# Optimization experiments

Measured on AMD Instinct MI355X. Metric: run time of the kernel, lower is better.

## Reference

```python
import jax, jax.numpy as jnp
import numpy as np

I1, I2, N = 256, 256, 256  # inp1_size, inp2_size, n_neurons
B = 4096
IN_DIM = (I1 + 1) * (I2 + 1)


def setup_inputs() -> dict:
    key = jax.random.key(0)
    k1, k2, kw1, kb1, kw2, kb2 = jax.random.split(key, 6)
    inp1 = jax.random.normal(k1, (B, I1), dtype=jnp.float32)
    inp2 = jax.random.normal(k2, (B, I2), dtype=jnp.float32)
    # Kaiming-uniform-ish init like torch nn.Linear
    lim1 = 1.0 / np.sqrt(IN_DIM)
    W1 = jax.random.uniform(kw1, (IN_DIM, N), jnp.float32, -lim1, lim1)
    b1 = jax.random.uniform(kb1, (N,), jnp.float32, -lim1, lim1)
    lim2 = 1.0 / np.sqrt(N)
    W2 = jax.random.uniform(kw2, (N, N), jnp.float32, -lim2, lim2)
    b2 = jax.random.uniform(kb2, (N,), jnp.float32, -lim2, lim2)
    return {"inp1": inp1, "inp2": inp2, "W1": W1, "b1": b1, "W2": W2, "b2": b2}


def reference(inp1, inp2, W1, b1, W2, b2):
    bsz = inp1.shape[0]
    ones = jnp.ones((bsz, 1), dtype=inp1.dtype)
    a = jnp.concatenate([inp1, ones], axis=-1)  # [B, I1+1]
    b = jnp.concatenate([inp2, ones], axis=-1)  # [B, I2+1]
    fusion = jnp.einsum('bi,bj->bij', a, b).reshape(bsz, -1)  # [B, (I1+1)*(I2+1)]
    h = jax.nn.relu(fusion @ W1 + b1)
    out = jax.nn.relu(h @ W2 + b2)
    return out
```

## Files before the change

kernel.cpp:

```cpp
#include <hip/hip_runtime.h>

#define DEVI __device__ __forceinline__

typedef __attribute__((ext_vector_type(4))) float f32x4;
typedef __attribute__((ext_vector_type(8))) short bf16x8;
typedef __attribute__((ext_vector_type(4))) unsigned int u32x4;

typedef __attribute__((address_space(3))) unsigned int lds_u32_t;
typedef __attribute__((address_space(1))) unsigned int glb_u32_t;

constexpr int BATCH = 4096;
constexpr int KTOT  = 66048;
constexpr size_t OFF_WPT  = 0;
constexpr size_t OFF_W2BT = 33816576;
constexpr size_t OFF_B1P  = OFF_W2BT + 131072;
constexpr size_t OFF_HF   = OFF_B1P + 1024;
constexpr size_t OFF_HB   = OFF_HF + 4194304;

DEVI unsigned int f2bf_u(float x) {
  unsigned int u = __float_as_uint(x);
  return (u + 0x7FFFu + ((u >> 16) & 1u)) >> 16;
}
DEVI unsigned int pack2(float a, float b) { return f2bf_u(a) | (f2bf_u(b) << 16); }

__global__ __launch_bounds__(256) void k_repack(const float* __restrict__ W1,
                                                unsigned short* __restrict__ wpt) {
  __shared__ float tile[64][65];
  int kt = blockIdx.x, nt = blockIdx.y, t = threadIdx.x;
  {
    int r = t >> 2, c4 = (t & 3) * 16;
    int kp = kt * 64 + r;
    int src;
    if (kp < 65536)      src = (kp >> 8) * 257 + (kp & 255);
    else if (kp < 65792) src = (kp - 65536) * 257 + 256;
    else                 src = kp;
    const float* rp = W1 + (size_t)src * 256 + nt * 64 + c4;
#pragma unroll
    for (int q = 0; q < 4; ++q) {
      f32x4 x = *(const f32x4*)(rp + q * 4);
#pragma unroll
      for (int e = 0; e < 4; ++e) tile[r][c4 + q * 4 + e] = x[e];
    }
  }
  __syncthreads();
  {
    int nl = t >> 2, kk = (t & 3) * 16;
    int n = nt * 64 + nl;
    u32x4 lo, hi;
#pragma unroll
    for (int m = 0; m < 4; ++m)
      lo[m] = pack2(tile[kk + 2 * m][nl], tile[kk + 2 * m + 1][nl]);
#pragma unroll
    for (int m = 0; m < 4; ++m)
      hi[m] = pack2(tile[kk + 8 + 2 * m][nl], tile[kk + 9 + 2 * m][nl]);
    unsigned short* dst = wpt + (size_t)n * KTOT + kt * 64 + kk;
    *(u32x4*)dst = lo;
    *(u32x4*)(dst + 8) = hi;
  }
}

__global__ __launch_bounds__(256) void k_misc(const float* __restrict__ W1,
                                              const float* __restrict__ b1,
                                              const float* __restrict__ W2,
                                              float* __restrict__ hf,
                                              unsigned short* __restrict__ w2bt,
                                              float* __restrict__ b1p) {
  int idx = blockIdx.x * 256 + threadIdx.x;
  hf[idx] = 0.f;
  if (idx < 65536) {
    int n2 = idx >> 8, n = idx & 255;
    w2bt[idx] = (unsigned short)f2bf_u(W2[n * 256 + n2]);
  }
  if (idx < 256) b1p[idx] = b1[idx] + W1[(size_t)66048 * 256 + idx];
}

DEVI void mfma_tiles(const char* A_lds, const char* W_lds, f32x4 (&acc)[8][4],
                     int lane, int wr, int wc) {
  int r16 = lane & 15;
  int kq = lane >> 4;
#pragma unroll
  for (int ks = 0; ks < 2; ++ks) {
    int kun = ks * 4 + kq;
    bf16x8 a[8];
#pragma unroll
    for (int rg = 0; rg < 8; ++rg) {
      int row = wr * 128 + rg * 16 + r16;
      a[rg] = *(const bf16x8*)(A_lds + row * 128 + ((kun ^ (row & 7)) << 4));
    }
#pragma unroll
    for (int cg = 0; cg < 4; ++cg) {
      int n = wc * 64 + cg * 16 + r16;
      bf16x8 bfr = *(const bf16x8*)(W_lds + n * 128 + ((kun ^ (n & 7)) << 4));
#pragma unroll
      for (int rg = 0; rg < 8; ++rg)
        acc[rg][cg] = __builtin_amdgcn_mfma_f32_16x16x32_bf16(a[rg], bfr, acc[rg][cg], 0, 0, 0);
    }
  }
}

DEVI void stage_w(const unsigned short* __restrict__ wpt, char* W_lds, int k0,
                  int w, int lane) {
#pragma unroll
  for (int sI = 0; sI < 4; ++sI) {
    int g = w * 256 + sI * 64 + lane;
    int n = g >> 3, u = g & 7;
    size_t gb = (size_t)n * (KTOT * 2) + (size_t)((k0 + ((u ^ (n & 7)) << 3)) * 2);
    __builtin_amdgcn_global_load_lds((const glb_u32_t*)((const char*)wpt + gb),
                                     (lds_u32_t*)(W_lds + g * 16), 16, 0, 0);
  }
}

__global__ __launch_bounds__(512) void k_main(const float* __restrict__ inp1,
                                              const float* __restrict__ inp2,
                                              const unsigned short* __restrict__ wpt,
                                              float* __restrict__ hf) {
  __shared__ u32x4 smem[4096];
  char* A_lds = (char*)smem;
  char* W_lds = (char*)smem + 32768;

  int lin = blockIdx.x;
  int xcd = lin & 7, slot = lin >> 3;
  int c = xcd + ((slot >> 4) << 3);
  int bblk = slot & 15;
  int b0 = bblk * 256;
  int i0 = c * 16;

  int t = threadIdx.x;
  int lane = t & 63, w = t >> 6;
  int wr = w >> 2, wc = w & 3;

  int row_a = t >> 1;
  int ub = (t & 1) * 4;

  const float* inp1_row = inp1 + (size_t)(b0 + row_a) * 256;
  const float* inp2_row = inp2 + (size_t)(b0 + row_a) * 256;

  f32x4 acc[8][4] = {};

  for (int js = 0; js < 4; ++js) {
    float v[32];
    {
      const f32x4* p = (const f32x4*)(inp2_row + js * 64 + ub * 8);
#pragma unroll
      for (int q = 0; q < 8; ++q) {
        f32x4 x = p[q];
#pragma unroll
        for (int e = 0; e < 4; ++e) v[q * 4 + e] = x[e];
      }
    }
    for (int ii = 0; ii < 16; ++ii) {
      int i = i0 + ii;
      float s = inp1_row[i];
#pragma unroll
      for (int uu = 0; uu < 4; ++uu) {
        int u = ub + uu;
        u32x4 pk;
#pragma unroll
        for (int m = 0; m < 4; ++m)
          pk[m] = pack2(v[uu * 8 + 2 * m] * s, v[uu * 8 + 2 * m + 1] * s);
        *(u32x4*)(A_lds + row_a * 128 + ((u ^ (row_a & 7)) << 4)) = pk;
      }
      stage_w(wpt, W_lds, i * 256 + js * 64, w, lane);
      __syncthreads();
      mfma_tiles(A_lds, W_lds, acc, lane, wr, wc);
      __syncthreads();
    }
  }

  if (c == 15) {
    for (int jt = 0; jt < 8; ++jt) {
#pragma unroll
      for (int uu = 0; uu < 4; ++uu) {
        int u = ub + uu;
        int koff = jt * 64 + u * 8;
        const float* src = (koff < 256) ? (inp1_row + koff) : (inp2_row + (koff - 256));
        f32x4 x0 = *(const f32x4*)src;
        f32x4 x1 = *(const f32x4*)(src + 4);
        u32x4 pk;
        pk[0] = pack2(x0[0], x0[1]);
        pk[1] = pack2(x0[2], x0[3]);
        pk[2] = pack2(x1[0], x1[1]);
        pk[3] = pack2(x1[2], x1[3]);
        *(u32x4*)(A_lds + row_a * 128 + ((u ^ (row_a & 7)) << 4)) = pk;
      }
      stage_w(wpt, W_lds, 65536 + jt * 64, w, lane);
      __syncthreads();
      mfma_tiles(A_lds, W_lds, acc, lane, wr, wc);
      __syncthreads();
    }
  }

#pragma unroll
  for (int rg = 0; rg < 8; ++rg)
#pragma unroll
    for (int cg = 0; cg < 4; ++cg) {
      int n = wc * 64 + cg * 16 + (lane & 15);
      int brow = b0 + wr * 128 + rg * 16 + (lane >> 4) * 4;
#pragma unroll
      for (int r = 0; r < 4; ++r)
        atomicAdd(hf + (size_t)(brow + r) * 256 + n, acc[rg][cg][r]);
    }
}

__global__ __launch_bounds__(256) void k_finalize(const float* __restrict__ hf,
                                                  const float* __restrict__ b1p,
                                                  unsigned short* __restrict__ hb) {
  int idx = blockIdx.x * 256 + threadIdx.x;
  float v = hf[idx] + b1p[idx & 255];
  hb[idx] = (unsigned short)f2bf_u(v > 0.f ? v : 0.f);
}

__global__ __launch_bounds__(256) void k_gemm2(const unsigned short* __restrict__ hb,
                                               const unsigned short* __restrict__ w2bt,
                                               const float* __restrict__ b2,
                                               float* __restrict__ out) {
  int b0 = blockIdx.x * 128, n0 = blockIdx.y * 128;
  int t = threadIdx.x, lane = t & 63, w = t >> 6;
  int wr = w >> 1, wc = w & 1;
  int r16 = lane & 15, k8 = (lane >> 4) * 8;
  f32x4 acc[4][4] = {};
  for (int ks = 0; ks < 8; ++ks) {
    int k = ks * 32 + k8;
    bf16x8 a[4], bb[4];
#pragma unroll
    for (int rg = 0; rg < 4; ++rg) {
      int b_ = b0 + wr * 64 + rg * 16 + r16;
      a[rg] = *(const bf16x8*)(hb + (size_t)b_ * 256 + k);
    }
#pragma unroll
    for (int cg = 0; cg < 4; ++cg) {
      int n2 = n0 + wc * 64 + cg * 16 + r16;
      bb[cg] = *(const bf16x8*)(w2bt + (size_t)n2 * 256 + k);
    }
#pragma unroll
    for (int rg = 0; rg < 4; ++rg)
#pragma unroll
      for (int cg = 0; cg < 4; ++cg)
        acc[rg][cg] = __builtin_amdgcn_mfma_f32_16x16x32_bf16(a[rg], bb[cg], acc[rg][cg], 0, 0, 0);
  }
#pragma unroll
  for (int rg = 0; rg < 4; ++rg)
#pragma unroll
    for (int cg = 0; cg < 4; ++cg) {
      int n2 = n0 + wc * 64 + cg * 16 + r16;
      float bias = b2[n2];
      int brow = b0 + wr * 64 + rg * 16 + (lane >> 4) * 4;
#pragma unroll
      for (int r = 0; r < 4; ++r) {
        float val = acc[rg][cg][r] + bias;
        out[(size_t)(brow + r) * 256 + n2] = val > 0.f ? val : 0.f;
      }
    }
}

extern "C" void kernel_launch(void* const* d_in, const int* in_sizes, int n_in,
                              void* d_out, int out_size, void* d_ws, size_t ws_size,
                              hipStream_t stream) {
  const float* inp1 = (const float*)d_in[0];
  const float* inp2 = (const float*)d_in[1];
  const float* W1   = (const float*)d_in[2];
  const float* b1   = (const float*)d_in[3];
  const float* W2   = (const float*)d_in[4];
  const float* b2   = (const float*)d_in[5];
  float* out = (float*)d_out;

  char* ws = (char*)d_ws;
  unsigned short* wpt  = (unsigned short*)(ws + OFF_WPT);
  unsigned short* w2bt = (unsigned short*)(ws + OFF_W2BT);
  float* b1p = (float*)(ws + OFF_B1P);
  float* hf  = (float*)(ws + OFF_HF);
  unsigned short* hb = (unsigned short*)(ws + OFF_HB);

  k_repack<<<dim3(1032, 4), 256, 0, stream>>>(W1, wpt);
  k_misc<<<4096, 256, 0, stream>>>(W1, b1, W2, hf, w2bt, b1p);
  k_main<<<256, 512, 0, stream>>>(inp1, inp2, wpt, hf);
  k_finalize<<<4096, 256, 0, stream>>>(hf, b1p, hb);
  k_gemm2<<<dim3(32, 2), 256, 0, stream>>>(hb, w2bt, b2, out);
}
```

Measured before the change: 338.0 us.

## Double-buffer LDS stages and spread tail K-chunks across blocks

```diff
diff --git a/kernel.cpp b/kernel.cpp
--- a/kernel.cpp
+++ b/kernel.cpp
@@ -9,7 +9,6 @@
 typedef __attribute__((address_space(3))) unsigned int lds_u32_t;
 typedef __attribute__((address_space(1))) unsigned int glb_u32_t;
 
-constexpr int BATCH = 4096;
 constexpr int KTOT  = 66048;
 constexpr size_t OFF_WPT  = 0;
 constexpr size_t OFF_W2BT = 33816576;
@@ -114,9 +113,8 @@
                                               const float* __restrict__ inp2,
                                               const unsigned short* __restrict__ wpt,
                                               float* __restrict__ hf) {
-  __shared__ u32x4 smem[4096];
-  char* A_lds = (char*)smem;
-  char* W_lds = (char*)smem + 32768;
+  __shared__ u32x4 smem[8192];
+  char* base = (char*)smem;
 
   int lin = blockIdx.x;
   int xcd = lin & 7, slot = lin >> 3;
@@ -135,59 +133,91 @@
   const float* inp1_row = inp1 + (size_t)(b0 + row_a) * 256;
   const float* inp2_row = inp2 + (size_t)(b0 + row_a) * 256;
 
+  float s1[16];
+  {
+    const f32x4* p = (const f32x4*)(inp1_row + i0);
+#pragma unroll
+    for (int q = 0; q < 4; ++q) {
+      f32x4 x = p[q];
+#pragma unroll
+      for (int e = 0; e < 4; ++e) s1[q * 4 + e] = x[e];
+    }
+  }
+
+  float v[32];
+  int js_cur = -1;
+  auto loadv = [&](int js) {
+    const f32x4* p = (const f32x4*)(inp2_row + js * 64 + ub * 8);
+#pragma unroll
+    for (int q = 0; q < 8; ++q) {
+      f32x4 x = p[q];
+#pragma unroll
+      for (int e = 0; e < 4; ++e) v[q * 4 + e] = x[e];
+    }
+    js_cur = js;
+  };
+
+  auto build_main = [&](char* A_lds, int ii) {
+    float s = s1[ii];
+#pragma unroll
+    for (int uu = 0; uu < 4; ++uu) {
+      int u = ub + uu;
+      u32x4 pk;
+#pragma unroll
+      for (int m = 0; m < 4; ++m)
+        pk[m] = pack2(v[uu * 8 + 2 * m] * s, v[uu * 8 + 2 * m + 1] * s);
+      *(u32x4*)(A_lds + row_a * 128 + ((u ^ (row_a & 7)) << 4)) = pk;
+    }
+  };
+
+  auto build_tail = [&](char* A_lds, int jt) {
+#pragma unroll
+    for (int uu = 0; uu < 4; ++uu) {
+      int u = ub + uu;
+      int koff = jt * 64 + u * 8;
+      const float* src = (koff < 256) ? (inp1_row + koff) : (inp2_row + (koff - 256));
+      f32x4 x0 = *(const f32x4*)src;
+      f32x4 x1 = *(const f32x4*)(src + 4);
+      u32x4 pk;
+      pk[0] = pack2(x0[0], x0[1]);
+      pk[1] = pack2(x0[2], x0[3]);
+      pk[2] = pack2(x1[0], x1[1]);
+      pk[3] = pack2(x1[2], x1[3]);
+      *(u32x4*)(A_lds + row_a * 128 + ((u ^ (row_a & 7)) << 4)) = pk;
+    }
+  };
+
   f32x4 acc[8][4] = {};
 
-  for (int js = 0; js < 4; ++js) {
-    float v[32];
-    {
-      const f32x4* p = (const f32x4*)(inp2_row + js * 64 + ub * 8);
-#pragma unroll
-      for (int q = 0; q < 8; ++q) {
-        f32x4 x = p[q];
-#pragma unroll
-        for (int e = 0; e < 4; ++e) v[q * 4 + e] = x[e];
+  const int NS = 64 + (c >= 8 ? 1 : 0);
+
+  loadv(0);
+  stage_w(wpt, base + 32768, i0 * 256, w, lane);
+  build_main(base, 0);
+  __syncthreads();
+
+  for (int s = 0; s < NS; ++s) {
+    int cur = s & 1, nxt = cur ^ 1;
+    char* A_cur = base + cur * 65536;
+    char* W_cur = base + cur * 65536 + 32768;
+    char* A_nxt = base + nxt * 65536;
+    char* W_nxt = base + nxt * 65536 + 32768;
+
+    int sn = s + 1;
+    if (sn < NS) {
+      if (sn < 64) {
+        int js = sn >> 4, ii = sn & 15;
+        stage_w(wpt, W_nxt, (i0 + ii) * 256 + js * 64, w, lane);
+        if (js != js_cur) loadv(js);
+        build_main(A_nxt, ii);
+      } else {
+        stage_w(wpt, W_nxt, 65536 + (c - 8) * 64, w, lane);
+        build_tail(A_nxt, c - 8);
       }
     }
-    for (int ii = 0; ii < 16; ++ii) {
-      int i = i0 + ii;
-      float s = inp1_row[i];
-#pragma unroll
-      for (int uu = 0; uu < 4; ++uu) {
-        int u = ub + uu;
-        u32x4 pk;
-#pragma unroll
-        for (int m = 0; m < 4; ++m)
-          pk[m] = pack2(v[uu * 8 + 2 * m] * s, v[uu * 8 + 2 * m + 1] * s);
-        *(u32x4*)(A_lds + row_a * 128 + ((u ^ (row_a & 7)) << 4)) = pk;
-      }
-      stage_w(wpt, W_lds, i * 256 + js * 64, w, lane);
-      __syncthreads();
-      mfma_tiles(A_lds, W_lds, acc, lane, wr, wc);
-      __syncthreads();
-    }
-  }
-
-  if (c == 15) {
-    for (int jt = 0; jt < 8; ++jt) {
-#pragma unroll
-      for (int uu = 0; uu < 4; ++uu) {
-        int u = ub + uu;
-        int koff = jt * 64 + u * 8;
-        const float* src = (koff < 256) ? (inp1_row + koff) : (inp2_row + (koff - 256));
-        f32x4 x0 = *(const f32x4*)src;
-        f32x4 x1 = *(const f32x4*)(src + 4);
-        u32x4 pk;
-        pk[0] = pack2(x0[0], x0[1]);
-        pk[1] = pack2(x0[2], x0[3]);
-        pk[2] = pack2(x1[0], x1[1]);
-        pk[3] = pack2(x1[2], x1[3]);
-        *(u32x4*)(A_lds + row_a * 128 + ((u ^ (row_a & 7)) << 4)) = pk;
-      }
-      stage_w(wpt, W_lds, 65536 + jt * 64, w, lane);
-      __syncthreads();
-      mfma_tiles(A_lds, W_lds, acc, lane, wr, wc);
-      __syncthreads();
-    }
+
+    mfma_tiles(A_cur, W_cur, acc, lane, wr, wc);
+    __syncthreads();
   }
 
 #pragma unroll
```

New measurement: 310.4 us. -8.2%, faster.

## Double-buffer k_main with smaller tiles, more blocks and split tail work

Applied to the files above, without the earlier changes.

```diff
diff --git a/kernel.cpp b/kernel.cpp
--- a/kernel.cpp
+++ b/kernel.cpp
@@ -9,7 +9,6 @@
 typedef __attribute__((address_space(3))) unsigned int lds_u32_t;
 typedef __attribute__((address_space(1))) unsigned int glb_u32_t;
 
-constexpr int BATCH = 4096;
 constexpr int KTOT  = 66048;
 constexpr size_t OFF_WPT  = 0;
 constexpr size_t OFF_W2BT = 33816576;
@@ -74,128 +73,138 @@
   if (idx < 256) b1p[idx] = b1[idx] + W1[(size_t)66048 * 256 + idx];
 }
 
-DEVI void mfma_tiles(const char* A_lds, const char* W_lds, f32x4 (&acc)[8][4],
-                     int lane, int wr, int wc) {
-  int r16 = lane & 15;
-  int kq = lane >> 4;
-#pragma unroll
-  for (int ks = 0; ks < 2; ++ks) {
-    int kun = ks * 4 + kq;
-    bf16x8 a[8];
-#pragma unroll
-    for (int rg = 0; rg < 8; ++rg) {
-      int row = wr * 128 + rg * 16 + r16;
-      a[rg] = *(const bf16x8*)(A_lds + row * 128 + ((kun ^ (row & 7)) << 4));
-    }
-#pragma unroll
-    for (int cg = 0; cg < 4; ++cg) {
-      int n = wc * 64 + cg * 16 + r16;
-      bf16x8 bfr = *(const bf16x8*)(W_lds + n * 128 + ((kun ^ (n & 7)) << 4));
-#pragma unroll
-      for (int rg = 0; rg < 8; ++rg)
-        acc[rg][cg] = __builtin_amdgcn_mfma_f32_16x16x32_bf16(a[rg], bfr, acc[rg][cg], 0, 0, 0);
-    }
-  }
-}
-
-DEVI void stage_w(const unsigned short* __restrict__ wpt, char* W_lds, int k0,
-                  int w, int lane) {
-#pragma unroll
-  for (int sI = 0; sI < 4; ++sI) {
-    int g = w * 256 + sI * 64 + lane;
-    int n = g >> 3, u = g & 7;
-    size_t gb = (size_t)n * (KTOT * 2) + (size_t)((k0 + ((u ^ (n & 7)) << 3)) * 2);
-    __builtin_amdgcn_global_load_lds((const glb_u32_t*)((const char*)wpt + gb),
-                                     (lds_u32_t*)(W_lds + g * 16), 16, 0, 0);
-  }
-}
-
-__global__ __launch_bounds__(512) void k_main(const float* __restrict__ inp1,
-                                              const float* __restrict__ inp2,
-                                              const unsigned short* __restrict__ wpt,
-                                              float* __restrict__ hf) {
-  __shared__ u32x4 smem[4096];
-  char* A_lds = (char*)smem;
-  char* W_lds = (char*)smem + 32768;
+__global__ __launch_bounds__(512, 4) void k_main(const float* __restrict__ inp1,
+                                                 const float* __restrict__ inp2,
+                                                 const unsigned short* __restrict__ wpt,
+                                                 float* __restrict__ hf) {
+  __shared__ char smem[49152];
 
   int lin = blockIdx.x;
   int xcd = lin & 7, slot = lin >> 3;
-  int c = xcd + ((slot >> 4) << 3);
-  int bblk = slot & 15;
-  int b0 = bblk * 256;
+  int c = xcd + ((slot >> 5) << 3);
+  int bblk = slot & 31;
+  int b0 = bblk * 128;
   int i0 = c * 16;
 
   int t = threadIdx.x;
   int lane = t & 63, w = t >> 6;
   int wr = w >> 2, wc = w & 3;
-
-  int row_a = t >> 1;
-  int ub = (t & 1) * 4;
+  int r16 = lane & 15, kun = lane >> 4;
+
+  int row_a = t >> 2;
+  int u_a = t & 3;
+  int a_waddr = row_a * 64 + ((u_a ^ ((row_a >> 1) & 3)) << 4);
 
   const float* inp1_row = inp1 + (size_t)(b0 + row_a) * 256;
   const float* inp2_row = inp2 + (size_t)(b0 + row_a) * 256;
 
-  f32x4 acc[8][4] = {};
-
-  for (int js = 0; js < 4; ++js) {
-    float v[32];
+  char* A0 = smem;             char* W0 = smem + 8192;
+  char* A1 = smem + 24576;     char* W1b = smem + 24576 + 8192;
+
+  float v[16];
+  auto loadv = [&](int js) {
+    const float* p = inp2_row + js * 64 + u_a * 8;
+#pragma unroll
+    for (int jw = 0; jw < 2; ++jw) {
+      f32x4 x0 = *(const f32x4*)(p + jw * 32);
+      f32x4 x1 = *(const f32x4*)(p + jw * 32 + 4);
+#pragma unroll
+      for (int e = 0; e < 4; ++e) { v[jw * 8 + e] = x0[e]; v[jw * 8 + 4 + e] = x1[e]; }
+    }
+  };
+
+  auto build_main = [&](char* A, int ii, int jw) {
+    float s = inp1_row[i0 + ii];
+    u32x4 pk;
+#pragma unroll
+    for (int m = 0; m < 4; ++m)
+      pk[m] = pack2(v[jw * 8 + 2 * m] * s, v[jw * 8 + 2 * m + 1] * s);
+    *(u32x4*)(A + a_waddr) = pk;
+  };
+
+  auto build_tail = [&](char* A) {
+    int koff = c * 32 + u_a * 8;
+    const float* src = (koff < 256) ? (inp1_row + koff) : (inp2_row + (koff - 256));
+    f32x4 x0 = *(const f32x4*)src;
+    f32x4 x1 = *(const f32x4*)(src + 4);
+    u32x4 pk;
+    pk[0] = pack2(x0[0], x0[1]);
+    pk[1] = pack2(x0[2], x0[3]);
+    pk[2] = pack2(x1[0], x1[1]);
+    pk[3] = pack2(x1[2], x1[3]);
+    *(u32x4*)(A + a_waddr) = pk;
+  };
+
+  auto stage = [&](char* W, int k0) {
+#pragma unroll
+    for (int sI = 0; sI < 2; ++sI) {
+      int g = w * 128 + sI * 64 + lane;
+      int n = g >> 2, u = g & 3;
+      size_t gb = (size_t)n * (KTOT * 2) +
+                  (size_t)((k0 + ((u ^ ((n >> 1) & 3)) << 3)) * 2);
+      __builtin_amdgcn_global_load_lds((const glb_u32_t*)((const char*)wpt + gb),
+                                       (lds_u32_t*)(W + g * 16), 16, 0, 0);
+    }
+  };
+
+  f32x4 acc[4][4] = {};
+
+  auto mfma_step = [&](const char* A, const char* W) {
+    bf16x8 a[4], b[4];
+#pragma unroll
+    for (int rg = 0; rg < 4; ++rg) {
+      int row = wr * 64 + rg * 16 + r16;
+      a[rg] = *(const bf16x8*)(A + row * 64 + ((kun ^ ((row >> 1) & 3)) << 4));
+    }
+#pragma unroll
+    for (int cg = 0; cg < 4; ++cg) {
+      int n = wc * 64 + cg * 16 + r16;
+      b[cg] = *(const bf16x8*)(W + n * 64 + ((kun ^ ((n >> 1) & 3)) << 4));
+    }
+#pragma unroll
+    for (int rg = 0; rg < 4; ++rg)
+#pragma unroll
+      for (int cg = 0; cg < 4; ++cg)
+        acc[rg][cg] = __builtin_amdgcn_mfma_f32_16x16x32_bf16(a[rg], b[cg], acc[rg][cg], 0, 0, 0);
+  };
+
+  loadv(0);
+  stage(W0, i0 * 256);
+  build_main(A0, 0, 0);
+  __syncthreads();
+
+  for (int s2 = 0; s2 < 64; ++s2) {
     {
-      const f32x4* p = (const f32x4*)(inp2_row + js * 64 + ub * 8);
-#pragma unroll
-      for (int q = 0; q < 8; ++q) {
-        f32x4 x = p[q];
-#pragma unroll
-        for (int e = 0; e < 4; ++e) v[q * 4 + e] = x[e];
+      int sn = 2 * s2 + 1;
+      int js = sn >> 5, ii = (sn >> 1) & 15;
+      stage(W1b, (i0 + ii) * 256 + js * 64 + 32);
+      build_main(A1, ii, 1);
+      mfma_step(A0, W0);
+      __syncthreads();
+    }
+    {
+      int sn = 2 * s2 + 2;
+      if (sn < 128) {
+        int js = sn >> 5, ii = (sn >> 1) & 15;
+        stage(W0, (i0 + ii) * 256 + js * 64);
+        if ((sn & 31) == 0) loadv(js);
+        build_main(A0, ii, 0);
+      } else {
+        stage(W0, 65536 + c * 32);
+        build_tail(A0);
       }
-    }
-    for (int ii = 0; ii < 16; ++ii) {
-      int i = i0 + ii;
-      float s = inp1_row[i];
-#pragma unroll
-      for (int uu = 0; uu < 4; ++uu) {
-        int u = ub + uu;
-        u32x4 pk;
-#pragma unroll
-        for (int m = 0; m < 4; ++m)
-          pk[m] = pack2(v[uu * 8 + 2 * m] * s, v[uu * 8 + 2 * m + 1] * s);
-        *(u32x4*)(A_lds + row_a * 128 + ((u ^ (row_a & 7)) << 4)) = pk;
-      }
-      stage_w(wpt, W_lds, i * 256 + js * 64, w, lane);
+      mfma_step(A1, W1b);
       __syncthreads();
-      mfma_tiles(A_lds, W_lds, acc, lane, wr, wc);
-      __syncthreads();
-    }
-  }
-
-  if (c == 15) {
-    for (int jt = 0; jt < 8; ++jt) {
-#pragma unroll
-      for (int uu = 0; uu < 4; ++uu) {
-        int u = ub + uu;
-        int koff = jt * 64 + u * 8;
-        const float* src = (koff < 256) ? (inp1_row + koff) : (inp2_row + (koff - 256));
-        f32x4 x0 = *(const f32x4*)src;
-        f32x4 x1 = *(const f32x4*)(src + 4);
-        u32x4 pk;
-        pk[0] = pack2(x0[0], x0[1]);
-        pk[1] = pack2(x0[2], x0[3]);
-        pk[2] = pack2(x1[0], x1[1]);
-        pk[3] = pack2(x1[2], x1[3]);
-        *(u32x4*)(A_lds + row_a * 128 + ((u ^ (row_a & 7)) << 4)) = pk;
-      }
-      stage_w(wpt, W_lds, 65536 + jt * 64, w, lane);
-      __syncthreads();
-      mfma_tiles(A_lds, W_lds, acc, lane, wr, wc);
-      __syncthreads();
-    }
-  }
-
-#pragma unroll
-  for (int rg = 0; rg < 8; ++rg)
-#pragma unroll
-    for (int cg = 0; cg < 4; ++cg) {
-      int n = wc * 64 + cg * 16 + (lane & 15);
-      int brow = b0 + wr * 128 + rg * 16 + (lane >> 4) * 4;
+    }
+  }
+  mfma_step(A0, W0);
+
+#pragma unroll
+  for (int rg = 0; rg < 4; ++rg)
+#pragma unroll
+    for (int cg = 0; cg < 4; ++cg) {
+      int n = wc * 64 + cg * 16 + r16;
+      int brow = b0 + wr * 64 + rg * 16 + kun * 4;
 #pragma unroll
       for (int r = 0; r < 4; ++r)
         atomicAdd(hf + (size_t)(brow + r) * 256 + n, acc[rg][cg][r]);
@@ -273,7 +282,7 @@
 
   k_repack<<<dim3(1032, 4), 256, 0, stream>>>(W1, wpt);
   k_misc<<<4096, 256, 0, stream>>>(W1, b1, W2, hf, w2bt, b1p);
-  k_main<<<256, 512, 0, stream>>>(inp1, inp2, wpt, hf);
+  k_main<<<512, 512, 0, stream>>>(inp1, inp2, wpt, hf);
   k_finalize<<<4096, 256, 0, stream>>>(hf, b1p, hb);
   k_gemm2<<<dim3(32, 2), 256, 0, stream>>>(hb, w2bt, b2, out);
 }
```

Result: faster. 324.9 us (-3.9%).

## Double-buffer main GEMM LDS tiles with four-phase MFMA pipeline and spread tail

Applied to the files above, without the earlier changes.

```diff
diff --git a/kernel.cpp b/kernel.cpp
--- a/kernel.cpp
+++ b/kernel.cpp
@@ -1,4 +1,5 @@
 #include <hip/hip_runtime.h>
+#include <hip/hip_bf16.h>
 
 #define DEVI __device__ __forceinline__
 
@@ -9,7 +10,6 @@
 typedef __attribute__((address_space(3))) unsigned int lds_u32_t;
 typedef __attribute__((address_space(1))) unsigned int glb_u32_t;
 
-constexpr int BATCH = 4096;
 constexpr int KTOT  = 66048;
 constexpr size_t OFF_WPT  = 0;
 constexpr size_t OFF_W2BT = 33816576;
@@ -17,11 +17,13 @@
 constexpr size_t OFF_HF   = OFF_B1P + 1024;
 constexpr size_t OFF_HB   = OFF_HF + 4194304;
 
-DEVI unsigned int f2bf_u(float x) {
-  unsigned int u = __float_as_uint(x);
-  return (u + 0x7FFFu + ((u >> 16) & 1u)) >> 16;
-}
-DEVI unsigned int pack2(float a, float b) { return f2bf_u(a) | (f2bf_u(b) << 16); }
+DEVI unsigned short f2bf(float x) {
+  __hip_bfloat16 h = __float2bfloat16(x);
+  return *reinterpret_cast<unsigned short*>(&h);
+}
+DEVI unsigned int pack2(float a, float b) {
+  return (unsigned int)f2bf(a) | ((unsigned int)f2bf(b) << 16);
+}
 
 __global__ __launch_bounds__(256) void k_repack(const float* __restrict__ W1,
                                                 unsigned short* __restrict__ wpt) {
@@ -69,137 +71,199 @@
   hf[idx] = 0.f;
   if (idx < 65536) {
     int n2 = idx >> 8, n = idx & 255;
-    w2bt[idx] = (unsigned short)f2bf_u(W2[n * 256 + n2]);
+    w2bt[idx] = f2bf(W2[n * 256 + n2]);
   }
   if (idx < 256) b1p[idx] = b1[idx] + W1[(size_t)66048 * 256 + idx];
 }
 
-DEVI void mfma_tiles(const char* A_lds, const char* W_lds, f32x4 (&acc)[8][4],
-                     int lane, int wr, int wc) {
-  int r16 = lane & 15;
-  int kq = lane >> 4;
-#pragma unroll
-  for (int ks = 0; ks < 2; ++ks) {
-    int kun = ks * 4 + kq;
-    bf16x8 a[8];
-#pragma unroll
-    for (int rg = 0; rg < 8; ++rg) {
-      int row = wr * 128 + rg * 16 + r16;
-      a[rg] = *(const bf16x8*)(A_lds + row * 128 + ((kun ^ (row & 7)) << 4));
-    }
+__global__ __launch_bounds__(512, 2) void k_main(const float* __restrict__ inp1,
+                                                 const float* __restrict__ inp2,
+                                                 const unsigned short* __restrict__ wpt,
+                                                 float* __restrict__ hf) {
+  __shared__ char smem[131072];
+
+  const int lin = blockIdx.x;
+  const int xcd = lin & 7, slot = lin >> 3;
+  const int c = xcd + ((slot >> 4) << 3);
+  const int b0 = (slot & 15) * 256;
+  const int i0 = c * 16;
+
+  const int t = threadIdx.x;
+  const int lane = t & 63, wid = t >> 6;
+  const int wrow = wid >> 2, wcol = wid & 3;
+  const int r16 = lane & 15, kq = lane >> 4;
+
+  const int brow_l = t >> 1;
+  const int bu0 = (t & 1) * 4;
+  const int brow7 = brow_l & 7;
+  const int a_wbase = brow_l * 128;
+  const bool bhalf0 = (brow_l < 128);
+  const float* inp1_row = inp1 + (size_t)(b0 + brow_l) * 256;
+  const float* inp2_row = inp2 + (size_t)(b0 + brow_l) * 256;
+
+  const unsigned short* wsrc[2];
+  int wdst[2];
+#pragma unroll
+  for (int q = 0; q < 2; ++q) {
+    int g = wid * 128 + q * 64 + lane;
+    int nl = g >> 3, up = g & 7, u = up ^ (nl & 7);
+    wsrc[q] = wpt + (size_t)nl * KTOT + u * 8;
+    wdst[q] = g * 16;
+  }
+
+  auto stageW = [&](char* Wreg, int h, int k0) {
+#pragma unroll
+    for (int q = 0; q < 2; ++q)
+      __builtin_amdgcn_global_load_lds(
+          (const glb_u32_t*)(wsrc[q] + (size_t)h * 128 * KTOT + k0),
+          (lds_u32_t*)(Wreg + h * 16384 + wdst[q]), 16, 0, 0);
+  };
+
+  float v2[32];
+  auto loadv2 = [&](int jw) {
+    const float* p = inp2_row + jw * 64 + bu0 * 8;
+#pragma unroll
+    for (int q8 = 0; q8 < 8; ++q8) {
+      f32x4 x = *(const f32x4*)(p + q8 * 4);
+#pragma unroll
+      for (int e = 0; e < 4; ++e) v2[q8 * 4 + e] = x[e];
+    }
+  };
+
+  auto buildA = [&](char* Areg, int ii) {
+    float s = inp1_row[i0 + ii];
+#pragma unroll
+    for (int uu = 0; uu < 4; ++uu) {
+      int u = bu0 + uu;
+      u32x4 pk;
+#pragma unroll
+      for (int m = 0; m < 4; ++m)
+        pk[m] = pack2(v2[uu * 8 + 2 * m] * s, v2[uu * 8 + 2 * m + 1] * s);
+      *(u32x4*)(Areg + a_wbase + ((u ^ brow7) << 4)) = pk;
+    }
+  };
+
+  auto buildTail = [&](char* Areg) {
+    const float* srcp = (c < 12) ? (inp1_row + (c - 8) * 64) : (inp2_row + (c - 12) * 64);
+#pragma unroll
+    for (int uu = 0; uu < 4; ++uu) {
+      int u = bu0 + uu;
+      f32x4 x0 = *(const f32x4*)(srcp + u * 8);
+      f32x4 x1 = *(const f32x4*)(srcp + u * 8 + 4);
+      u32x4 pk;
+      pk[0] = pack2(x0[0], x0[1]); pk[1] = pack2(x0[2], x0[3]);
+      pk[2] = pack2(x1[0], x1[1]); pk[3] = pack2(x1[2], x1[3]);
+      *(u32x4*)(Areg + a_wbase + ((u ^ brow7) << 4)) = pk;
+    }
+  };
+
+  f32x4 acc[8][4] = {};
+  bf16x8 af[4][2];
+  bf16x8 bfr[2][2];
+
+  auto readA = [&](const char* Areg, int rgh) {
+#pragma unroll
+    for (int r = 0; r < 4; ++r) {
+      int row = wrow * 128 + (rgh * 4 + r) * 16 + r16;
+      int rb = row * 128, r7 = row & 7;
+#pragma unroll
+      for (int ks = 0; ks < 2; ++ks)
+        af[r][ks] = *(const bf16x8*)(Areg + rb + (((ks * 4 + kq) ^ r7) << 4));
+    }
+  };
+  auto readB = [&](const char* Wreg, int cgp) {
+#pragma unroll
+    for (int cl = 0; cl < 2; ++cl) {
+      int n = wcol * 64 + (cgp * 2 + cl) * 16 + r16;
+      int nb = n * 128, n7 = n & 7;
+#pragma unroll
+      for (int ks = 0; ks < 2; ++ks)
+        bfr[cl][ks] = *(const bf16x8*)(Wreg + nb + (((ks * 4 + kq) ^ n7) << 4));
+    }
+  };
+
+#define MFMA_Q(rgh, cgp)                                                        \
+  do {                                                                          \
+    __builtin_amdgcn_s_setprio(1);                                              \
+    _Pragma("unroll") for (int ks = 0; ks < 2; ++ks)                            \
+      _Pragma("unroll") for (int r = 0; r < 4; ++r)                             \
+        _Pragma("unroll") for (int cl = 0; cl < 2; ++cl)                        \
+          acc[(rgh)*4 + r][(cgp)*2 + cl] = __builtin_amdgcn_mfma_f32_16x16x32_bf16( \
+              af[r][ks], bfr[cl][ks], acc[(rgh)*4 + r][(cgp)*2 + cl], 0, 0, 0); \
+    __builtin_amdgcn_s_setprio(0);                                              \
+  } while (0)
+
+#define PHASE_SYNC()                                            \
+  do {                                                          \
+    asm volatile("" ::: "memory");                              \
+    __builtin_amdgcn_s_barrier();                               \
+    asm volatile("s_waitcnt lgkmcnt(0)" ::: "memory");          \
+    __builtin_amdgcn_sched_barrier(0);                          \
+  } while (0)
+
+#define PHASE_END()                                             \
+  do {                                                          \
+    asm volatile("" ::: "memory");                              \
+    __builtin_amdgcn_s_barrier();                               \
+  } while (0)
+
+  const int NT = 64 + (c >= 8 ? 1 : 0);
+
+  loadv2(0);
+  stageW(smem + 32768, 0, i0 * 256);
+  stageW(smem + 32768, 1, i0 * 256);
+  buildA(smem, 0);
+  asm volatile("s_waitcnt vmcnt(0) lgkmcnt(0)" ::: "memory");
+  __syncthreads();
+
+  for (int tt = 0; tt < NT; ++tt) {
+    char* Acur = smem + (tt & 1) * 65536;
+    char* Wcur = Acur + 32768;
+    char* Anxt = smem + (((tt & 1) ^ 1)) * 65536;
+    char* Wnxt = Anxt + 32768;
+    const int sn = tt + 1;
+    const bool hn = sn < NT;
+    const bool tail_n = hn && (sn == 64);
+    const int ii_n = sn & 15, jw_n = sn >> 4;
+    const int k0n = tail_n ? (65536 + (c - 8) * 64)
+                           : ((i0 + ii_n) * 256 + jw_n * 64);
+
+    readA(Acur, 0); readB(Wcur, 0);
+    if (hn) stageW(Wnxt, 0, k0n);
+    PHASE_SYNC(); MFMA_Q(0, 0); PHASE_END();
+
+    readB(Wcur, 1);
+    if (hn) stageW(Wnxt, 1, k0n);
+    PHASE_SYNC(); MFMA_Q(0, 1); PHASE_END();
+
+    readA(Acur, 1); readB(Wcur, 0);
+    if (hn && !tail_n && (sn & 15) == 0) loadv2(jw_n);
+    if (hn && bhalf0) {
+      if (!tail_n) buildA(Anxt, ii_n); else buildTail(Anxt);
+    }
+    PHASE_SYNC(); MFMA_Q(1, 0); PHASE_END();
+
+    readB(Wcur, 1);
+    if (hn && !bhalf0) {
+      if (!tail_n) buildA(Anxt, ii_n); else buildTail(Anxt);
+    }
+    asm volatile("s_waitcnt vmcnt(0)" ::: "memory");
+    PHASE_SYNC(); MFMA_Q(1, 1); PHASE_END();
+  }
+
+#pragma unroll
+  for (int rg = 0; rg < 8; ++rg)
 #pragma unroll
     for (int cg = 0; cg < 4; ++cg) {
-      int n = wc * 64 + cg * 16 + r16;
-      bf16x8 bfr = *(const bf16x8*)(W_lds + n * 128 + ((kun ^ (n & 7)) << 4));
-#pragma unroll
-      for (int rg = 0; rg < 8; ++rg)
-        acc[rg][cg] = __builtin_amdgcn_mfma_f32_16x16x32_bf16(a[rg], bfr, acc[rg][cg], 0, 0, 0);
-    }
-  }
-}
-
-DEVI void stage_w(const unsigned short* __restrict__ wpt, char* W_lds, int k0,
-                  int w, int lane) {
-#pragma unroll
-  for (int sI = 0; sI < 4; ++sI) {
-    int g = w * 256 + sI * 64 + lane;
-    int n = g >> 3, u = g & 7;
-    size_t gb = (size_t)n * (KTOT * 2) + (size_t)((k0 + ((u ^ (n & 7)) << 3)) * 2);
-    __builtin_amdgcn_global_load_lds((const glb_u32_t*)((const char*)wpt + gb),
-                                     (lds_u32_t*)(W_lds + g * 16), 16, 0, 0);
-  }
-}
-
-__global__ __launch_bounds__(512) void k_main(const float* __restrict__ inp1,
-                                              const float* __restrict__ inp2,
-                                              const unsigned short* __restrict__ wpt,
-                                              float* __restrict__ hf) {
-  __shared__ u32x4 smem[4096];
-  char* A_lds = (char*)smem;
-  char* W_lds = (char*)smem + 32768;
-
-  int lin = blockIdx.x;
-  int xcd = lin & 7, slot = lin >> 3;
-  int c = xcd + ((slot >> 4) << 3);
-  int bblk = slot & 15;
-  int b0 = bblk * 256;
-  int i0 = c * 16;
-
-  int t = threadIdx.x;
-  int lane = t & 63, w = t >> 6;
-  int wr = w >> 2, wc = w & 3;
-
-  int row_a = t >> 1;
-  int ub = (t & 1) * 4;
-
-  const float* inp1_row = inp1 + (size_t)(b0 + row_a) * 256;
-  const float* inp2_row = inp2 + (size_t)(b0 + row_a) * 256;
-
-  f32x4 acc[8][4] = {};
-
-  for (int js = 0; js < 4; ++js) {
-    float v[32];
-    {
-      const f32x4* p = (const f32x4*)(inp2_row + js * 64 + ub * 8);
-#pragma unroll
-      for (int q = 0; q < 8; ++q) {
-        f32x4 x = p[q];
-#pragma unroll
-        for (int e = 0; e < 4; ++e) v[q * 4 + e] = x[e];
-      }
-    }
-    for (int ii = 0; ii < 16; ++ii) {
-      int i = i0 + ii;
-      float s = inp1_row[i];
-#pragma unroll
-      for (int uu = 0; uu < 4; ++uu) {
-        int u = ub + uu;
-        u32x4 pk;
-#pragma unroll
-        for (int m = 0; m < 4; ++m)
-          pk[m] = pack2(v[uu * 8 + 2 * m] * s, v[uu * 8 + 2 * m + 1] * s);
-        *(u32x4*)(A_lds + row_a * 128 + ((u ^ (row_a & 7)) << 4)) = pk;
-      }
-      stage_w(wpt, W_lds, i * 256 + js * 64, w, lane);
-      __syncthreads();
-      mfma_tiles(A_lds, W_lds, acc, lane, wr, wc);
-      __syncthreads();
-    }
-  }
-
-  if (c == 15) {
-    for (int jt = 0; jt < 8; ++jt) {
-#pragma unroll
-      for (int uu = 0; uu < 4; ++uu) {
-        int u = ub + uu;
-        int koff = jt * 64 + u * 8;
-        const float* src = (koff < 256) ? (inp1_row + koff) : (inp2_row + (koff - 256));
-        f32x4 x0 = *(const f32x4*)src;
-        f32x4 x1 = *(const f32x4*)(src + 4);
-        u32x4 pk;
-        pk[0] = pack2(x0[0], x0[1]);
-        pk[1] = pack2(x0[2], x0[3]);
-        pk[2] = pack2(x1[0], x1[1]);
-        pk[3] = pack2(x1[2], x1[3]);
-        *(u32x4*)(A_lds + row_a * 128 + ((u ^ (row_a & 7)) << 4)) = pk;
-      }
-      stage_w(wpt, W_lds, 65536 + jt * 64, w, lane);
-      __syncthreads();
-      mfma_tiles(A_lds, W_lds, acc, lane, wr, wc);
-      __syncthreads();
-    }
-  }
-
-#pragma unroll
-  for (int rg = 0; rg < 8; ++rg)
-#pragma unroll
-    for (int cg = 0; cg < 4; ++cg) {
-      int n = wc * 64 + cg * 16 + (lane & 15);
-      int brow = b0 + wr * 128 + rg * 16 + (lane >> 4) * 4;
+      int n = wcol * 64 + cg * 16 + r16;
+      int br = b0 + wrow * 128 + rg * 16 + kq * 4;
 #pragma unroll
       for (int r = 0; r < 4; ++r)
-        atomicAdd(hf + (size_t)(brow + r) * 256 + n, acc[rg][cg][r]);
-    }
+        atomicAdd(hf + (size_t)(br + r) * 256 + n, acc[rg][cg][r]);
+    }
+#undef MFMA_Q
+#undef PHASE_SYNC
+#undef PHASE_END
 }
 
 __global__ __launch_bounds__(256) void k_finalize(const float* __restrict__ hf,
@@ -207,7 +271,7 @@
                                                   unsigned short* __restrict__ hb) {
   int idx = blockIdx.x * 256 + threadIdx.x;
   float v = hf[idx] + b1p[idx & 255];
-  hb[idx] = (unsigned short)f2bf_u(v > 0.f ? v : 0.f);
+  hb[idx] = f2bf(v > 0.f ? v : 0.f);
 }
 
 __global__ __launch_bounds__(256) void k_gemm2(const unsigned short* __restrict__ hb,
```

After: 505.7 us. 1.5x slower.
